# Optimization experiments

Measured on AMD Instinct MI355X. Metric: run time of the kernel, lower is better.

## Reference

```python
import jax, jax.numpy as jnp
import numpy as np

BOX = 8.0  # side length of the box points are sampled in
N_POINTS = 12288
N_BINS_TARGET = 10


def setup_inputs() -> dict:
    key = jax.random.key(0)
    k1, k2 = jax.random.split(key)
    pc = jax.random.uniform(k1, (N_POINTS, 3), dtype=jnp.float32) * BOX
    target_rdf = jax.random.uniform(k2, (N_BINS_TARGET,), dtype=jnp.float32) * 2.0
    return {"reconstructed_pc": pc, "target_rdf": target_rdf, "r_max": 10, "dr": 1.0}


def _calculate_rdf(pc, r_max, dr):
    # pc: [N, 3]. r_max, dr are static Python scalars.
    n = pc.shape[0]
    nbins = int(round(float(r_max) / float(dr)))  # len(arange(0, r_max+dr, dr)) - 1
    # Pairwise Euclidean distances via the Gram-matrix trick (same math as torch.cdist p=2).
    sq = jnp.sum(pc * pc, axis=1)                               # [N]
    d2 = sq[:, None] + sq[None, :] - 2.0 * (pc @ pc.T)          # [N, N]
    d = jnp.sqrt(jnp.maximum(d2, 0.0)).ravel()                  # [N*N]
    # torch.histc(bins=nbins, min=0, max=r_max): uniform bins, max value inclusive in last bin.
    idx = jnp.clip(jnp.floor(d / dr).astype(jnp.int32), 0, nbins - 1)
    w = (d <= r_max).astype(jnp.float32)                        # d >= 0 always holds
    hist = jax.ops.segment_sum(w, idx, num_segments=nbins)      # [nbins]
    r_mid = (jnp.arange(nbins, dtype=jnp.float32) + 0.5) * dr
    density = n / (4.0 / 3.0 * jnp.pi * float(r_max) ** 3)
    ideal_counts = 4.0 * jnp.pi * r_mid ** 2 * dr * density * n
    rdf = hist / ideal_counts
    rdf = jnp.where(jnp.isnan(rdf), 0.0, rdf)
    return rdf, r_mid


def reference(reconstructed_pc, target_rdf, r_max, dr):
    rdf, _ = _calculate_rdf(reconstructed_pc, r_max, dr)
    m = min(int(target_rdf.shape[0]), int(rdf.shape[0]))
    diff = rdf[:m] - target_rdf[:m]
    return jnp.mean(diff * diff)
```

## Files before the change

kernel.cpp:

```cpp
#include <hip/hip_runtime.h>


#define BLOCK    256
#define IBLK     4
#define ITILE    (BLOCK * IBLK)
#define JCH      64
#define DJC      (ITILE / JCH)
#define NB       10
#define SLOT     16
#define FP32_SAT 16777216u

typedef float f32x2 __attribute__((ext_vector_type(2)));

__device__ __forceinline__ int pre_rows(int k, int njc) {
    return k * njc - (DJC / 2) * k * (k - 1);
}

template <bool STRADDLE>
__device__ __forceinline__ void jloop(const float4* __restrict__ sj,
                                      const f32x2* sqiv, const f32x2* m2xv,
                                      const f32x2* m2yv, const f32x2* m2zv,
                                      const int* iidx, int jbase,
                                      unsigned int* c)
{
    #pragma unroll
    for (int jc0 = 0; jc0 < JCH; jc0 += 8) {
        unsigned long long cnt = 0ull;
        #pragma unroll
        for (int jj = 0; jj < 8; ++jj) {
            const int j = jc0 + jj;
            float4 p = sj[j];
            const f32x2 pw = {p.w, p.w}, px = {p.x, p.x};
            const f32x2 py = {p.y, p.y}, pz = {p.z, p.z};
            #pragma unroll
            for (int rp = 0; rp < IBLK / 2; ++rp) {
                f32x2 d2 = sqiv[rp] + pw;
                d2 = __builtin_elementwise_fma(m2xv[rp], px, d2);
                d2 = __builtin_elementwise_fma(m2yv[rp], py, d2);
                d2 = __builtin_elementwise_fma(m2zv[rp], pz, d2);
                float d2a = d2.x, d2b = d2.y;
                if (STRADDLE) {
                    d2a = (jbase + j > iidx[2 * rp])     ? d2a : 3.0e30f;
                    d2b = (jbase + j > iidx[2 * rp + 1]) ? d2b : 3.0e30f;
                }
                float da = __builtin_amdgcn_sqrtf(d2a);
                float db = __builtin_amdgcn_sqrtf(d2b);
                unsigned int ba = min((unsigned int)da, 10u);
                unsigned int bb = min((unsigned int)db, 10u);
                cnt += 1ull << (ba * 6u);
                cnt += 1ull << (bb * 6u);
            }
        }
        #pragma unroll
        for (int k = 0; k < NB; ++k)
            c[k] += (unsigned int)(cnt >> (6 * k)) & 63u;
    }
}

__global__ __launch_bounds__(BLOCK) void rdf_hist_kernel(
    const float* __restrict__ pc, const int* __restrict__ rmaxp,
    const float* __restrict__ drp, unsigned int* __restrict__ part,
    int n, int nI, int njc)
{
    __shared__ float4 sj[JCH];
    __shared__ unsigned int sacc[NB];

    const int tid = threadIdx.x;
    const int bid = (int)blockIdx.x;

    const float a  = (float)(DJC / 2);
    const float bq = (float)njc + a;
    float disc = fmaxf(bq * bq - 4.0f * a * (float)bid, 0.0f);
    int k = (int)((bq - sqrtf(disc)) / (2.0f * a));
    k = max(0, min(k, nI - 1));
    while (k > 0 && pre_rows(k, njc) > bid) --k;
    while (k + 1 < nI && pre_rows(k + 1, njc) <= bid) ++k;
    const int jc    = (bid - pre_rows(k, njc)) + DJC * k;
    const int ibase = k * ITILE;
    const int jbase = jc * JCH;

    const float inv_dr = 1.0f / (*drp);

    float jx = -3.0e4f, jy = -3.0e4f, jz = -3.0e4f;
    if (tid < JCH) {
        const int j = jbase + tid;
        if (j < n) { jx = pc[3*j]; jy = pc[3*j+1]; jz = pc[3*j+2]; }
    }
    float rx[IBLK], ry[IBLK], rz[IBLK];
    int iidx[IBLK];
    #pragma unroll
    for (int r = 0; r < IBLK; ++r) {
        const int i = ibase + tid + BLOCK * r;
        iidx[r] = i;
        rx[r] = 3.0e4f; ry[r] = 3.0e4f; rz[r] = 3.0e4f;
        if (i < n) { rx[r] = pc[3*i]; ry[r] = pc[3*i+1]; rz[r] = pc[3*i+2]; }
    }

    if (tid < NB) sacc[tid] = 0u;
    if (tid < JCH) {
        const float x = jx * inv_dr, y = jy * inv_dr, z = jz * inv_dr;
        sj[tid] = make_float4(x, y, z, x*x + y*y + z*z);
    }
    f32x2 sqiv[IBLK/2], m2xv[IBLK/2], m2yv[IBLK/2], m2zv[IBLK/2];
    #pragma unroll
    for (int r = 0; r < IBLK; ++r) {
        const float x = rx[r] * inv_dr, y = ry[r] * inv_dr, z = rz[r] * inv_dr;
        const float sq = x*x + y*y + z*z;
        sqiv[r/2][r&1] = sq;
        m2xv[r/2][r&1] = -2.f * x;
        m2yv[r/2][r&1] = -2.f * y;
        m2zv[r/2][r&1] = -2.f * z;
    }

    __syncthreads();

    unsigned int c[NB];
    #pragma unroll
    for (int q = 0; q < NB; ++q) c[q] = 0u;

    if (jbase < ibase + ITILE)
        jloop<true >(sj, sqiv, m2xv, m2yv, m2zv, iidx, jbase, c);
    else
        jloop<false>(sj, sqiv, m2xv, m2yv, m2zv, iidx, jbase, c);

    #pragma unroll
    for (int q = 0; q < NB; ++q) {
        unsigned int s = c[q];
        #pragma unroll
        for (int m = 32; m >= 1; m >>= 1) s += (unsigned int)__shfl_xor((int)s, m, 64);
        c[q] = s;
    }
    if ((tid & 63) == 0) {
        #pragma unroll
        for (int q = 0; q < NB; ++q) atomicAdd(&sacc[q], c[q]);
    }
    __syncthreads();
    if (tid < NB) part[bid * SLOT + tid] = sacc[tid];
}

__global__ __launch_bounds__(BLOCK) void rdf_reduce_loss_kernel(
    const unsigned int* __restrict__ part, const float* __restrict__ target,
    const int* __restrict__ rmaxp, const float* __restrict__ drp,
    float* __restrict__ out, int n, int mt, int nblocks)
{
    __shared__ unsigned int sacc[NB];
    const int tid = threadIdx.x;
    if (tid < NB) sacc[tid] = 0u;
    __syncthreads();

    unsigned int a[NB];
    #pragma unroll
    for (int q = 0; q < NB; ++q) a[q] = 0u;
    for (int s = tid; s < nblocks; s += BLOCK) {
        #pragma unroll
        for (int q = 0; q < NB; ++q) a[q] += part[s * SLOT + q];
    }
    #pragma unroll
    for (int q = 0; q < NB; ++q) {
        unsigned int s = a[q];
        #pragma unroll
        for (int m = 32; m >= 1; m >>= 1) s += (unsigned int)__shfl_xor((int)s, m, 64);
        if ((tid & 63) == 0) atomicAdd(&sacc[q], s);
    }
    __syncthreads();

    if (tid == 0) {
        const float PI = 3.14159265358979323846f;
        const float rmax = (float)(*rmaxp);
        const float dr   = *drp;
        int nbins = (int)roundf(rmax / dr);
        if (nbins > NB) nbins = NB;
        const float density = (float)n / (4.0f / 3.0f * PI * rmax * rmax * rmax);
        const int m = (mt < nbins) ? mt : nbins;
        float acc = 0.0f;
        for (int b = 0; b < m; ++b) {
            unsigned int hb = 2u * sacc[b] + ((b == 0) ? (unsigned int)n : 0u);
            if (hb > FP32_SAT) hb = FP32_SAT;
            float r_mid = ((float)b + 0.5f) * dr;
            float ideal = 4.0f * PI * r_mid * r_mid * dr * density * (float)n;
            float rdf  = (ideal != 0.0f) ? ((float)hb / ideal) : 0.0f;
            float diff = rdf - target[b];
            acc = fmaf(diff, diff, acc);
        }
        out[0] = acc / (float)m;
    }
}

extern "C" void kernel_launch(void* const* d_in, const int* in_sizes, int n_in,
                              void* d_out, int out_size, void* d_ws, size_t ws_size,
                              hipStream_t stream)
{
    const float* pc     = (const float*)d_in[0];
    const float* target = (const float*)d_in[1];
    const int*   rmaxp  = (const int*)d_in[2];
    const float* drp    = (const float*)d_in[3];
    const int n  = in_sizes[0] / 3;
    const int mt = in_sizes[1];

    unsigned int* part = (unsigned int*)d_ws;
    const int nI  = (n + ITILE - 1) / ITILE;
    const int njc = (n + JCH - 1) / JCH;
    const int nblocks = nI * njc - (DJC / 2) * nI * (nI - 1);

    rdf_hist_kernel<<<nblocks, BLOCK, 0, stream>>>(pc, rmaxp, drp, part, n, nI, njc);
    rdf_reduce_loss_kernel<<<1, BLOCK, 0, stream>>>(part, target, rmaxp, drp,
                                                    (float*)d_out, n, mt, nblocks);
}
```

Before: 39.74 us.

## Precompute scaled j-points in a prep kernel and read them from global memory

Adds a prep kernel that scales every point by 1/dr and stores (x,y,z,|p|^2) as float4 in workspace. The histogram kernel drops its shared-memory staging and the __syncthreads-dependent j-chunk load, reading the j-points straight from global memory with uniform addresses (likely scalar or broadcast loads). This removes redundant per-block preprocessing and LDS traffic. In exchange it adds a kernel launch, and the j-point loads now hit cache instead of LDS.

```diff
diff --git a/kernel.cpp b/kernel.cpp
--- a/kernel.cpp
+++ b/kernel.cpp
@@ -16,8 +16,20 @@
     return k * njc - (DJC / 2) * k * (k - 1);
 }
 
+__global__ __launch_bounds__(256) void rdf_prep_kernel(
+    const float* __restrict__ pc, const float* __restrict__ drp,
+    float4* __restrict__ prepped, int n, int ntot)
+{
+    const int i = (int)blockIdx.x * 256 + (int)threadIdx.x;
+    if (i >= ntot) return;
+    const float inv_dr = 1.0f / (*drp);
+    float x = -3.0e4f, y = -3.0e4f, z = -3.0e4f;
+    if (i < n) { x = pc[3*i] * inv_dr; y = pc[3*i+1] * inv_dr; z = pc[3*i+2] * inv_dr; }
+    prepped[i] = make_float4(x, y, z, x*x + y*y + z*z);
+}
+
 template <bool STRADDLE>
-__device__ __forceinline__ void jloop(const float4* __restrict__ sj,
+__device__ __forceinline__ void jloop(const float4* __restrict__ pj,
                                       const f32x2* sqiv, const f32x2* m2xv,
                                       const f32x2* m2yv, const f32x2* m2zv,
                                       const int* iidx, int jbase,
@@ -29,7 +41,7 @@
         #pragma unroll
         for (int jj = 0; jj < 8; ++jj) {
             const int j = jc0 + jj;
-            float4 p = sj[j];
+            float4 p = pj[j];
             const f32x2 pw = {p.w, p.w}, px = {p.x, p.x};
             const f32x2 py = {p.y, p.y}, pz = {p.z, p.z};
             #pragma unroll
@@ -58,11 +70,10 @@
 }
 
 __global__ __launch_bounds__(BLOCK) void rdf_hist_kernel(
-    const float* __restrict__ pc, const int* __restrict__ rmaxp,
+    const float* __restrict__ pc, const float4* __restrict__ prepped,
     const float* __restrict__ drp, unsigned int* __restrict__ part,
     int n, int nI, int njc)
 {
-    __shared__ float4 sj[JCH];
     __shared__ unsigned int sacc[NB];
 
     const int tid = threadIdx.x;
@@ -81,11 +92,6 @@
 
     const float inv_dr = 1.0f / (*drp);
 
-    float jx = -3.0e4f, jy = -3.0e4f, jz = -3.0e4f;
-    if (tid < JCH) {
-        const int j = jbase + tid;
-        if (j < n) { jx = pc[3*j]; jy = pc[3*j+1]; jz = pc[3*j+2]; }
-    }
     float rx[IBLK], ry[IBLK], rz[IBLK];
     int iidx[IBLK];
     #pragma unroll
@@ -97,10 +103,7 @@
     }
 
     if (tid < NB) sacc[tid] = 0u;
-    if (tid < JCH) {
-        const float x = jx * inv_dr, y = jy * inv_dr, z = jz * inv_dr;
-        sj[tid] = make_float4(x, y, z, x*x + y*y + z*z);
-    }
+
     f32x2 sqiv[IBLK/2], m2xv[IBLK/2], m2yv[IBLK/2], m2zv[IBLK/2];
     #pragma unroll
     for (int r = 0; r < IBLK; ++r) {
@@ -118,10 +121,12 @@
     #pragma unroll
     for (int q = 0; q < NB; ++q) c[q] = 0u;
 
+    const float4* __restrict__ pj = prepped + jbase;
+
     if (jbase < ibase + ITILE)
-        jloop<true >(sj, sqiv, m2xv, m2yv, m2zv, iidx, jbase, c);
+        jloop<true >(pj, sqiv, m2xv, m2yv, m2zv, iidx, jbase, c);
     else
-        jloop<false>(sj, sqiv, m2xv, m2yv, m2zv, iidx, jbase, c);
+        jloop<false>(pj, sqiv, m2xv, m2yv, m2zv, iidx, jbase, c);
 
     #pragma unroll
     for (int q = 0; q < NB; ++q) {
@@ -197,12 +202,17 @@
     const int n  = in_sizes[0] / 3;
     const int mt = in_sizes[1];
 
-    unsigned int* part = (unsigned int*)d_ws;
-    const int nI  = (n + ITILE - 1) / ITILE;
-    const int njc = (n + JCH - 1) / JCH;
+    const int nI   = (n + ITILE - 1) / ITILE;
+    const int njc  = (n + JCH - 1) / JCH;
+    const int njTot = njc * JCH;
     const int nblocks = nI * njc - (DJC / 2) * nI * (nI - 1);
 
-    rdf_hist_kernel<<<nblocks, BLOCK, 0, stream>>>(pc, rmaxp, drp, part, n, nI, njc);
+    float4*       prepped = (float4*)d_ws;
+    size_t        part_off = ((size_t)njTot * sizeof(float4) + 255) & ~(size_t)255;
+    unsigned int* part     = (unsigned int*)((char*)d_ws + part_off);
+
+    rdf_prep_kernel<<<(njTot + 255) / 256, 256, 0, stream>>>(pc, drp, prepped, n, njTot);
+    rdf_hist_kernel<<<nblocks, BLOCK, 0, stream>>>(pc, prepped, drp, part, n, nI, njc);
     rdf_reduce_loss_kernel<<<1, BLOCK, 0, stream>>>(part, target, rmaxp, drp,
                                                     (float*)d_out, n, mt, nblocks);
 }
```

Result: slower. 43.85 us (+10.3%).
